# Kernel optimization log

Hardware: AMD Instinct MI355X
Metric: run time of the kernel (lower is better)

Reference implementation:

```python
import jax, jax.numpy as jnp
import numpy as np

DIM = 1024
N_HEADS = 16
B, T = 2, 2048


def setup_inputs() -> dict:
    key = jax.random.key(0)
    ks = jax.random.split(key, 9)
    s = 1.0 / np.sqrt(DIM)
    return {
        "x": jax.random.normal(ks[0], (B, T, DIM), dtype=jnp.float32),
        "Wq": jax.random.normal(ks[1], (DIM, DIM), dtype=jnp.float32) * s,
        "bq": jnp.zeros((DIM,), dtype=jnp.float32),
        "Wk": jax.random.normal(ks[2], (DIM, DIM), dtype=jnp.float32) * s,
        "bk": jnp.zeros((DIM,), dtype=jnp.float32),
        "Wv": jax.random.normal(ks[3], (DIM, DIM), dtype=jnp.float32) * s,
        "bv": jnp.zeros((DIM,), dtype=jnp.float32),
        "Wo": jax.random.normal(ks[4], (DIM, DIM), dtype=jnp.float32) * s,
        "bo": jnp.zeros((DIM,), dtype=jnp.float32),
    }


def reference(x, Wq, bq, Wk, bk, Wv, bv, Wo, bo):
    Bv, Tv, d = x.shape
    n = N_HEADS
    hd = d // n
    # projections (torch Linear: x @ W.T + b)
    Q = x @ Wq.T + bq
    K = x @ Wk.T + bk
    V = x @ Wv.T + bv
    # [B, n, T, hd]
    Q = Q.reshape(Bv, Tv, n, hd).transpose(0, 2, 1, 3)
    K = K.reshape(Bv, Tv, n, hd).transpose(0, 2, 1, 3)
    V = V.reshape(Bv, Tv, n, hd).transpose(0, 2, 1, 3)
    # NOTE: original scales by full model dim, not head dim
    scale = 1.0 / jnp.sqrt(jnp.asarray(d, dtype=x.dtype))
    scores = jnp.einsum('bnqd,bnkd->bnqk', Q, K) * scale
    causal = jnp.tril(jnp.ones((Tv, Tv), dtype=bool))
    scores = jnp.where(causal, scores, jnp.asarray(-jnp.inf, dtype=scores.dtype))
    attn = jax.nn.softmax(scores, axis=-1)
    out = jnp.einsum('bnqk,bnkd->bnqd', attn, V)
    out = out.transpose(0, 2, 1, 3).reshape(Bv, Tv, d)
    return out @ Wo.T + bo
```

## Files before the change

kernel.cpp:

```cpp
#include <hip/hip_runtime.h>
#include <math.h>

#define DIMN 1024
#define NH 16
#define HD 64
#define BATCH 2
#define SEQ 2048
#define MROWS (BATCH*SEQ)

typedef unsigned short u16;
typedef unsigned int u32;
typedef __attribute__((ext_vector_type(8))) short bf16x8;
typedef __attribute__((ext_vector_type(4))) float f32x4;

__device__ __forceinline__ u16 f2bf(float f) {
    unsigned u = __float_as_uint(f);
    u += 0x7FFF + ((u >> 16) & 1);
    return (u16)(u >> 16);
}
__device__ __forceinline__ float bf2f(u16 s) {
    return __uint_as_float(((unsigned)s) << 16);
}

#define GLOADLDS16(g, s)                                                     \
    __builtin_amdgcn_global_load_lds(                                        \
        (const __attribute__((address_space(1))) void*)(g),                  \
        (__attribute__((address_space(3))) void*)(s), 16, 0, 0)

__global__ __launch_bounds__(256)
void split_hilo(const float* __restrict__ src, u16* __restrict__ h,
                u16* __restrict__ l, int n4)
{
    int i = blockIdx.x * 256 + threadIdx.x;
    if (i >= n4) return;
    float4 v = ((const float4*)src)[i];
    ushort4 hv, lv;
    hv.x = f2bf(v.x); lv.x = f2bf(v.x - bf2f(hv.x));
    hv.y = f2bf(v.y); lv.y = f2bf(v.y - bf2f(hv.y));
    hv.z = f2bf(v.z); lv.z = f2bf(v.z - bf2f(hv.z));
    hv.w = f2bf(v.w); lv.w = f2bf(v.w - bf2f(hv.w));
    ((ushort4*)h)[i] = hv;
    ((ushort4*)l)[i] = lv;
}

__global__ __launch_bounds__(256)
void split4_hilo(const float* __restrict__ s0, const float* __restrict__ s1,
                 const float* __restrict__ s2, const float* __restrict__ s3,
                 u16* __restrict__ h0, u16* __restrict__ l0,
                 u16* __restrict__ h1, u16* __restrict__ l1,
                 u16* __restrict__ h2, u16* __restrict__ l2,
                 u16* __restrict__ h3, u16* __restrict__ l3, int n4)
{
    const float* src; u16* h; u16* l;
    switch (blockIdx.z) {
        case 0: src = s0; h = h0; l = l0; break;
        case 1: src = s1; h = h1; l = l1; break;
        case 2: src = s2; h = h2; l = l2; break;
        default: src = s3; h = h3; l = l3; break;
    }
    int i = blockIdx.x * 256 + threadIdx.x;
    if (i >= n4) return;
    float4 v = ((const float4*)src)[i];
    ushort4 hv, lv;
    hv.x = f2bf(v.x); lv.x = f2bf(v.x - bf2f(hv.x));
    hv.y = f2bf(v.y); lv.y = f2bf(v.y - bf2f(hv.y));
    hv.z = f2bf(v.z); lv.z = f2bf(v.z - bf2f(hv.z));
    hv.w = f2bf(v.w); lv.w = f2bf(v.w - bf2f(hv.w));
    ((ushort4*)h)[i] = hv;
    ((ushort4*)l)[i] = lv;
}

template<int NF, bool QKV>
__global__ __launch_bounds__(256)
void mfma_gemm(const u16* __restrict__ Ah, const u16* __restrict__ Al,
               const u16* __restrict__ Wh0, const u16* __restrict__ Wl0,
               const u16* __restrict__ Wh1, const u16* __restrict__ Wl1,
               const u16* __restrict__ Wh2, const u16* __restrict__ Wl2,
               const float* __restrict__ b0, const float* __restrict__ b1,
               const float* __restrict__ b2,
               u16* __restrict__ Qh, u16* __restrict__ Ql,
               u16* __restrict__ Kh, u16* __restrict__ Kl,
               float* __restrict__ Vw, float* __restrict__ Yout)
{
    constexpr int BM = 128;
    constexpr int BN = NF * 32;
    constexpr int BK = 32;
    __shared__ u16 AhS[BM*BK], AlS[BM*BK], WhS[BN*BK], WlS[BN*BK];

    const u16* Wh = Wh0; const u16* Wl = Wl0; const float* bias = b0;
    if (QKV) {
        if (blockIdx.z == 1)      { Wh = Wh1; Wl = Wl1; bias = b1; }
        else if (blockIdx.z == 2) { Wh = Wh2; Wl = Wl2; bias = b2; }
    }

    const int tid  = threadIdx.x;
    const int lane = tid & 63;
    const int wid  = tid >> 6;
    const int wr   = wid >> 1;
    const int wc   = wid & 1;

    const int m0 = blockIdx.x * BM;
    const int n0 = blockIdx.y * BN;

    const int srow = lane >> 2;
    const int skc  = (lane & 3) << 3;
    const int c0 = wid * 2, c1 = wid * 2 + 1;
    const size_t aoffg0 = (size_t)(m0 + c0*16 + srow) * DIMN + skc;
    const size_t aoffg1 = (size_t)(m0 + c1*16 + srow) * DIMN + skc;
    const size_t woffg0 = (size_t)(n0 + c0*16 + srow) * DIMN + skc;
    const size_t woffg1 = (size_t)(n0 + c1*16 + srow) * DIMN + skc;
    const bool doW = (c0 < BN/16);

    f32x4 acc[4][NF];
    #pragma unroll
    for (int m = 0; m < 4; ++m)
        #pragma unroll
        for (int n = 0; n < NF; ++n)
            acc[m][n] = (f32x4){0.f, 0.f, 0.f, 0.f};

    const int fr = lane & 15;
    const int fq = lane >> 4;
    const int aoff = (wr*64 + fr) * BK + fq*8;
    const int boff = (wc*(NF*16) + fr) * BK + fq*8;

    for (int k0 = 0; k0 < DIMN; k0 += BK) {
        GLOADLDS16(Ah + aoffg0 + k0, &AhS[c0*512]);
        GLOADLDS16(Ah + aoffg1 + k0, &AhS[c1*512]);
        GLOADLDS16(Al + aoffg0 + k0, &AlS[c0*512]);
        GLOADLDS16(Al + aoffg1 + k0, &AlS[c1*512]);
        if (doW) {
            GLOADLDS16(Wh + woffg0 + k0, &WhS[c0*512]);
            GLOADLDS16(Wh + woffg1 + k0, &WhS[c1*512]);
            GLOADLDS16(Wl + woffg0 + k0, &WlS[c0*512]);
            GLOADLDS16(Wl + woffg1 + k0, &WlS[c1*512]);
        }
        __syncthreads();

        bf16x8 ah[4], al[4], bh[NF], bl[NF];
        #pragma unroll
        for (int m = 0; m < 4; ++m) {
            ah[m] = *(const bf16x8*)&AhS[aoff + m*16*BK];
            al[m] = *(const bf16x8*)&AlS[aoff + m*16*BK];
        }
        #pragma unroll
        for (int n = 0; n < NF; ++n) {
            bh[n] = *(const bf16x8*)&WhS[boff + n*16*BK];
            bl[n] = *(const bf16x8*)&WlS[boff + n*16*BK];
        }
        #pragma unroll
        for (int m = 0; m < 4; ++m)
            #pragma unroll
            for (int n = 0; n < NF; ++n) {
                acc[m][n] = __builtin_amdgcn_mfma_f32_16x16x32_bf16(ah[m], bh[n], acc[m][n], 0, 0, 0);
                acc[m][n] = __builtin_amdgcn_mfma_f32_16x16x32_bf16(ah[m], bl[n], acc[m][n], 0, 0, 0);
                acc[m][n] = __builtin_amdgcn_mfma_f32_16x16x32_bf16(al[m], bh[n], acc[m][n], 0, 0, 0);
            }
        __syncthreads();
    }

    #pragma unroll
    for (int n = 0; n < NF; ++n) {
        const int col = n0 + wc*(NF*16) + n*16 + fr;
        const float bv = bias[col];
        #pragma unroll
        for (int m = 0; m < 4; ++m) {
            #pragma unroll
            for (int j = 0; j < 4; ++j) {
                const int row = m0 + wr*64 + m*16 + fq*4 + j;
                float v = acc[m][n][j] + bv;
                if (QKV) {
                    const int b_ = row >> 11, t = row & (SEQ - 1);
                    const int hh = col >> 6, d = col & 63;
                    const size_t rb = (((size_t)b_*NH + hh)*SEQ + t)*HD;
                    if (blockIdx.z == 0) {
                        v *= 0.03125f;
                        u16 hv = f2bf(v), lv = f2bf(v - bf2f(hv));
                        Qh[rb + d] = hv; Ql[rb + d] = lv;
                    } else if (blockIdx.z == 1) {
                        u16 hv = f2bf(v), lv = f2bf(v - bf2f(hv));
                        const int ds = d ^ ((t & 7) << 3);
                        Kh[rb + ds] = hv; Kl[rb + ds] = lv;
                    } else {
                        Vw[rb + d] = v;
                    }
                } else {
                    Yout[(size_t)row*DIMN + col] = v;
                }
            }
        }
    }
}

__global__ __launch_bounds__(256)
void convV(const float* __restrict__ Vw, u16* __restrict__ Vth, u16* __restrict__ Vtl)
{
    __shared__ float Vs[64][68];
    const int tid = threadIdx.x;
    const int bh = blockIdx.y;
    const int t0 = blockIdx.x * 64;
    const float* src = Vw + ((size_t)bh*SEQ + t0)*HD;
    #pragma unroll
    for (int k = 0; k < 4; ++k) {
        int f4 = tid + k*256;
        int r = f4 >> 4, c4 = (f4 & 15) << 2;
        *(float4*)&Vs[r][c4] = *(const float4*)(src + (size_t)r*HD + c4);
    }
    __syncthreads();
    const int d  = tid >> 2;
    const int q2 = (tid & 3) << 4;
    u16* oh = Vth + ((size_t)bh*HD + d)*SEQ + t0;
    u16* ol = Vtl + ((size_t)bh*HD + d)*SEQ + t0;
    #pragma unroll
    for (int p = 0; p < 4; ++p) {
        const int lt = q2 + p*4;
        const int t_sw = (lt & 32) | ((((lt >> 3) & 3) ^ (d & 3)) << 3) | (lt & 7);
        ushort4 hv, lv; float v;
        v = Vs[lt + 0][d]; hv.x = f2bf(v); lv.x = f2bf(v - bf2f(hv.x));
        v = Vs[lt + 1][d]; hv.y = f2bf(v); lv.y = f2bf(v - bf2f(hv.y));
        v = Vs[lt + 2][d]; hv.z = f2bf(v); lv.z = f2bf(v - bf2f(hv.z));
        v = Vs[lt + 3][d]; hv.w = f2bf(v); lv.w = f2bf(v - bf2f(hv.w));
        *(ushort4*)(oh + t_sw) = hv;
        *(ushort4*)(ol + t_sw) = lv;
    }
}

__global__ __launch_bounds__(256)
void attn_mfma(const u16* __restrict__ Qhg, const u16* __restrict__ Qlg,
               const u16* __restrict__ Khg, const u16* __restrict__ Klg,
               const u16* __restrict__ Vthg, const u16* __restrict__ Vtlg,
               u16* __restrict__ AH, u16* __restrict__ AL)
{
    __shared__ u16 KVS[2][4][2048];
    __shared__ u16 PhS[4][640];
    __shared__ u16 PlS[4][640];

    const int tid  = threadIdx.x;
    const int lane = tid & 63;
    const int w    = tid >> 6;
    const int fr   = lane & 15;
    const int fq   = lane >> 4;
    const int bh   = blockIdx.y;
    const int b_   = bh >> 4;
    const int h    = bh & 15;

    auto stage = [&](int buf, int kt2) {
        u16* dst = &KVS[buf][w][0];
        if (w < 2) {
            const u16* g = (w == 0 ? Khg : Klg) +
                ((size_t)bh*SEQ + (size_t)kt2*32 + (lane>>3))*HD + ((lane&7)<<3);
            #pragma unroll
            for (int i = 0; i < 4; ++i)
                GLOADLDS16(g + (size_t)i*8*HD, dst + i*512);
        } else {
            const u16* g = (w == 2 ? Vthg : Vtlg) +
                ((size_t)bh*HD + (lane>>2))*SEQ + (size_t)kt2*32 + ((lane&3)<<3);
            #pragma unroll
            for (int i = 0; i < 4; ++i)
                GLOADLDS16(g + (size_t)i*16*SEQ, dst + i*512);
        }
    };

    #pragma unroll 1
    for (int pass = 0; pass < 2; ++pass) {
        const int qt   = pass ? (31 - blockIdx.x) : blockIdx.x;
        const int qabs = qt*64 + w*16 + fr;
        const int nt   = 2*qt + 2;

        bf16x8 qh[2], ql[2];
        {
            const size_t qrow = ((size_t)bh*SEQ + qabs)*HD;
            #pragma unroll
            for (int ks = 0; ks < 2; ++ks) {
                qh[ks] = *(const bf16x8*)&Qhg[qrow + ks*32 + (fq<<3)];
                ql[ks] = *(const bf16x8*)&Qlg[qrow + ks*32 + (fq<<3)];
            }
        }

        f32x4 o[4];
        #pragma unroll
        for (int md = 0; md < 4; ++md) o[md] = (f32x4){0.f,0.f,0.f,0.f};
        float mrun = -INFINITY, lrun = 0.f;

        __syncthreads();
        stage(0, 0);
        int cur = 0;

        for (int kt = 0; kt < nt; ++kt) {
            __syncthreads();
            if (kt + 1 < nt) stage(cur ^ 1, kt + 1);

            f32x4 s0 = (f32x4){0.f,0.f,0.f,0.f};
            f32x4 s1 = (f32x4){0.f,0.f,0.f,0.f};
            __builtin_amdgcn_s_setprio(1);
            #pragma unroll
            for (int ks = 0; ks < 2; ++ks) {
                const int sl = (((ks*4 + fq) ^ (fr & 7)) << 3);
                bf16x8 a0h = *(const bf16x8*)&KVS[cur][0][fr*64 + sl];
                bf16x8 a0l = *(const bf16x8*)&KVS[cur][1][fr*64 + sl];
                bf16x8 a1h = *(const bf16x8*)&KVS[cur][0][(16+fr)*64 + sl];
                bf16x8 a1l = *(const bf16x8*)&KVS[cur][1][(16+fr)*64 + sl];
                s0 = __builtin_amdgcn_mfma_f32_16x16x32_bf16(a0h, qh[ks], s0, 0,0,0);
                s0 = __builtin_amdgcn_mfma_f32_16x16x32_bf16(a0h, ql[ks], s0, 0,0,0);
                s0 = __builtin_amdgcn_mfma_f32_16x16x32_bf16(a0l, qh[ks], s0, 0,0,0);
                s1 = __builtin_amdgcn_mfma_f32_16x16x32_bf16(a1h, qh[ks], s1, 0,0,0);
                s1 = __builtin_amdgcn_mfma_f32_16x16x32_bf16(a1h, ql[ks], s1, 0,0,0);
                s1 = __builtin_amdgcn_mfma_f32_16x16x32_bf16(a1l, qh[ks], s1, 0,0,0);
            }
            __builtin_amdgcn_s_setprio(0);

            const int kb = kt*32 + fq*4;
            #pragma unroll
            for (int j = 0; j < 4; ++j) {
                if (kb + j      > qabs) s0[j] = -INFINITY;
                if (kb + 16 + j > qabs) s1[j] = -INFINITY;
            }

            float pm = fmaxf(fmaxf(fmaxf(s0[0],s0[1]), fmaxf(s0[2],s0[3])),
                             fmaxf(fmaxf(s1[0],s1[1]), fmaxf(s1[2],s1[3])));
            pm = fmaxf(pm, __shfl_xor(pm, 16));
            pm = fmaxf(pm, __shfl_xor(pm, 32));

            if (!__all(pm - mrun <= 8.0f)) {
                const float mnew = fmaxf(mrun, pm);
                const float fac  = __expf(mrun - mnew);
                lrun *= fac;
                #pragma unroll
                for (int md = 0; md < 4; ++md) {
                    o[md][0] *= fac; o[md][1] *= fac;
                    o[md][2] *= fac; o[md][3] *= fac;
                }
                mrun = mnew;
            }
            float p[8];
            #pragma unroll
            for (int j = 0; j < 4; ++j) {
                p[j]   = __expf(s0[j] - mrun);
                p[4+j] = __expf(s1[j] - mrun);
            }
            float ls = ((p[0]+p[1]) + (p[2]+p[3])) + ((p[4]+p[5]) + (p[6]+p[7]));
            ls += __shfl_xor(ls, 16);
            ls += __shfl_xor(ls, 32);
            lrun += ls;

            u16 ph[8], pl[8];
            #pragma unroll
            for (int i = 0; i < 8; ++i) {
                ph[i] = f2bf(p[i]);
                pl[i] = f2bf(p[i] - bf2f(ph[i]));
            }
            {
                const int pb = fr*40 + fq*4;
                uint2 w0, w1;
                w0.x = (u32)ph[0] | ((u32)ph[1] << 16);
                w0.y = (u32)ph[2] | ((u32)ph[3] << 16);
                w1.x = (u32)ph[4] | ((u32)ph[5] << 16);
                w1.y = (u32)ph[6] | ((u32)ph[7] << 16);
                *(uint2*)&PhS[w][pb]      = w0;
                *(uint2*)&PhS[w][pb + 16] = w1;
                w0.x = (u32)pl[0] | ((u32)pl[1] << 16);
                w0.y = (u32)pl[2] | ((u32)pl[3] << 16);
                w1.x = (u32)pl[4] | ((u32)pl[5] << 16);
                w1.y = (u32)pl[6] | ((u32)pl[7] << 16);
                *(uint2*)&PlS[w][pb]      = w0;
                *(uint2*)&PlS[w][pb + 16] = w1;
            }

            bf16x8 bph = *(const bf16x8*)&PhS[w][fr*40 + (fq<<3)];
            bf16x8 bpl = *(const bf16x8*)&PlS[w][fr*40 + (fq<<3)];
            __builtin_amdgcn_s_setprio(1);
            #pragma unroll
            for (int md = 0; md < 4; ++md) {
                const int vsl = ((fq ^ (fr & 3)) << 3);
                bf16x8 avh = *(const bf16x8*)&KVS[cur][2][(md*16+fr)*32 + vsl];
                bf16x8 avl = *(const bf16x8*)&KVS[cur][3][(md*16+fr)*32 + vsl];
                o[md] = __builtin_amdgcn_mfma_f32_16x16x32_bf16(avh, bph, o[md], 0,0,0);
                o[md] = __builtin_amdgcn_mfma_f32_16x16x32_bf16(avh, bpl, o[md], 0,0,0);
                o[md] = __builtin_amdgcn_mfma_f32_16x16x32_bf16(avl, bph, o[md], 0,0,0);
            }
            __builtin_amdgcn_s_setprio(0);
            cur ^= 1;
        }

        const float inv = 1.f / lrun;
        const size_t ob = ((size_t)b_*SEQ + qabs)*DIMN + h*64;
        #pragma unroll
        for (int md = 0; md < 4; ++md) {
            #pragma unroll
            for (int pr = 0; pr < 2; ++pr) {
                const int d0 = md*16 + fq*4 + pr*2;
                const float v0 = o[md][pr*2]   * inv;
                const float v1 = o[md][pr*2+1] * inv;
                u16 h0 = f2bf(v0), l0 = f2bf(v0 - bf2f(h0));
                u16 h1 = f2bf(v1), l1 = f2bf(v1 - bf2f(h1));
                *(u32*)&AH[ob + d0] = (u32)h0 | ((u32)h1 << 16);
                *(u32*)&AL[ob + d0] = (u32)l0 | ((u32)l1 << 16);
            }
        }
    }
}

extern "C" void kernel_launch(void* const* d_in, const int* in_sizes, int n_in,
                              void* d_out, int out_size, void* d_ws, size_t ws_size,
                              hipStream_t stream)
{
    const float* x  = (const float*)d_in[0];
    const float* Wq = (const float*)d_in[1];
    const float* bq = (const float*)d_in[2];
    const float* Wk = (const float*)d_in[3];
    const float* bk = (const float*)d_in[4];
    const float* Wv = (const float*)d_in[5];
    const float* bv = (const float*)d_in[6];
    const float* Wo = (const float*)d_in[7];
    const float* bo = (const float*)d_in[8];
    float* out = (float*)d_out;

    const size_t NX = (size_t)MROWS * DIMN;
    const size_t NW = (size_t)DIMN * DIMN;

    u16* Xh  = (u16*)d_ws;
    u16* Xl  = Xh  + NX;
    u16* WhQ = Xl  + NX;  u16* WlQ = WhQ + NW;
    u16* WhK = WlQ + NW;  u16* WlK = WhK + NW;
    u16* WhV = WlK + NW;  u16* WlV = WhV + NW;
    u16* WhO = WlV + NW;  u16* WlO = WhO + NW;
    u16* Qh  = WlO + NW;
    u16* Ql  = Qh + NX;
    u16* Kh  = Ql + NX;
    u16* Kl  = Kh + NX;
    u16* Vth = Kl + NX;
    u16* Vtl = Vth + NX;
    float* Vw = (float*)(Vtl + NX);
    u16* AH = Xh;
    u16* AL = Xl;

    const int n4x = (int)(NX / 4);
    const int n4w = (int)(NW / 4);
    split_hilo<<<n4x/256, 256, 0, stream>>>(x, Xh, Xl, n4x);
    dim3 gs(n4w/256, 1, 4);
    split4_hilo<<<gs, 256, 0, stream>>>(Wq, Wk, Wv, Wo,
                                        WhQ, WlQ, WhK, WlK, WhV, WlV, WhO, WlO, n4w);

    dim3 gq(MROWS/128, DIMN/128, 3);
    mfma_gemm<4, true><<<gq, 256, 0, stream>>>(Xh, Xl, WhQ, WlQ, WhK, WlK, WhV, WlV,
                                               bq, bk, bv, Qh, Ql, Kh, Kl, Vw, nullptr);

    dim3 gv(SEQ / 64, BATCH * NH);
    convV<<<gv, 256, 0, stream>>>(Vw, Vth, Vtl);

    dim3 ga(16, BATCH * NH);
    attn_mfma<<<ga, 256, 0, stream>>>(Qh, Ql, Kh, Kl, Vth, Vtl, AH, AL);

    dim3 gp(MROWS/128, DIMN/64, 1);
    mfma_gemm<2, false><<<gp, 256, 0, stream>>>(AH, AL, WhO, WlO, nullptr, nullptr,
                                                nullptr, nullptr, bo, nullptr, nullptr,
                                                nullptr, nullptr, nullptr, nullptr,
                                                nullptr, out);
}
```

Baseline: 339.2 us.

## Merge split kernels, fold log2e into Q scale, remap attention blocks for XCD locality

The separate x and weight hi/lo split kernels become one five-slice launch, removing a kernel launch. The Q scale now includes log2(e), so softmax uses exp2f directly and the deferred-rescale threshold is adjusted to match. Attention block indices are remapped so blocks sharing a batch-head land on the same XCD, aiming at better L2 reuse of K/V. The bf16 conversion now uses the HIP intrinsic, and the merged split grid launches many idle blocks for the smaller weight slices.

```diff
diff --git a/kernel.cpp b/kernel.cpp
--- a/kernel.cpp
+++ b/kernel.cpp
@@ -1,4 +1,5 @@
 #include <hip/hip_runtime.h>
+#include <hip/hip_bf16.h>
 #include <math.h>
 
 #define DIMN 1024
@@ -13,10 +14,12 @@
 typedef __attribute__((ext_vector_type(8))) short bf16x8;
 typedef __attribute__((ext_vector_type(4))) float f32x4;
 
+#define QSCALE 0.0450842200279f
+#define DEFER_THR 11.5415603372f
+
 __device__ __forceinline__ u16 f2bf(float f) {
-    unsigned u = __float_as_uint(f);
-    u += 0x7FFF + ((u >> 16) & 1);
-    return (u16)(u >> 16);
+    __hip_bfloat16 h = __float2bfloat16(f);
+    return *reinterpret_cast<u16*>(&h);
 }
 __device__ __forceinline__ float bf2f(u16 s) {
     return __uint_as_float(((unsigned)s) << 16);
@@ -28,35 +31,23 @@
         (__attribute__((address_space(3))) void*)(s), 16, 0, 0)
 
 __global__ __launch_bounds__(256)
-void split_hilo(const float* __restrict__ src, u16* __restrict__ h,
-                u16* __restrict__ l, int n4)
-{
-    int i = blockIdx.x * 256 + threadIdx.x;
-    if (i >= n4) return;
-    float4 v = ((const float4*)src)[i];
-    ushort4 hv, lv;
-    hv.x = f2bf(v.x); lv.x = f2bf(v.x - bf2f(hv.x));
-    hv.y = f2bf(v.y); lv.y = f2bf(v.y - bf2f(hv.y));
-    hv.z = f2bf(v.z); lv.z = f2bf(v.z - bf2f(hv.z));
-    hv.w = f2bf(v.w); lv.w = f2bf(v.w - bf2f(hv.w));
-    ((ushort4*)h)[i] = hv;
-    ((ushort4*)l)[i] = lv;
-}
-
-__global__ __launch_bounds__(256)
-void split4_hilo(const float* __restrict__ s0, const float* __restrict__ s1,
+void split5_hilo(const float* __restrict__ s0, const float* __restrict__ s1,
                  const float* __restrict__ s2, const float* __restrict__ s3,
+                 const float* __restrict__ s4,
                  u16* __restrict__ h0, u16* __restrict__ l0,
                  u16* __restrict__ h1, u16* __restrict__ l1,
                  u16* __restrict__ h2, u16* __restrict__ l2,
-                 u16* __restrict__ h3, u16* __restrict__ l3, int n4)
+                 u16* __restrict__ h3, u16* __restrict__ l3,
+                 u16* __restrict__ h4, u16* __restrict__ l4,
+                 int n4x, int n4w)
 {
-    const float* src; u16* h; u16* l;
+    const float* src; u16* h; u16* l; int n4;
     switch (blockIdx.z) {
-        case 0: src = s0; h = h0; l = l0; break;
-        case 1: src = s1; h = h1; l = l1; break;
-        case 2: src = s2; h = h2; l = l2; break;
-        default: src = s3; h = h3; l = l3; break;
+        case 0: src = s0; h = h0; l = l0; n4 = n4x; break;
+        case 1: src = s1; h = h1; l = l1; n4 = n4w; break;
+        case 2: src = s2; h = h2; l = l2; n4 = n4w; break;
+        case 3: src = s3; h = h3; l = l3; n4 = n4w; break;
+        default: src = s4; h = h4; l = l4; n4 = n4w; break;
     }
     int i = blockIdx.x * 256 + threadIdx.x;
     if (i >= n4) return;
@@ -173,7 +164,7 @@
                     const int hh = col >> 6, d = col & 63;
                     const size_t rb = (((size_t)b_*NH + hh)*SEQ + t)*HD;
                     if (blockIdx.z == 0) {
-                        v *= 0.03125f;
+                        v *= QSCALE;
                         u16 hv = f2bf(v), lv = f2bf(v - bf2f(hv));
                         Qh[rb + d] = hv; Ql[rb + d] = lv;
                     } else if (blockIdx.z == 1) {
@@ -239,9 +230,14 @@
     const int w    = tid >> 6;
     const int fr   = lane & 15;
     const int fq   = lane >> 4;
-    const int bh   = blockIdx.y;
-    const int b_   = bh >> 4;
-    const int h    = bh & 15;
+
+    const int lin = blockIdx.y * 16 + blockIdx.x;
+    const int xcd = lin & 7;
+    const int idx = lin >> 3;
+    const int bh  = (xcd << 2) | (idx & 3);
+    const int qtp = idx >> 2;
+    const int b_  = bh >> 4;
+    const int h   = bh & 15;
 
     auto stage = [&](int buf, int kt2) {
         u16* dst = &KVS[buf][w][0];
@@ -262,7 +258,7 @@
 
     #pragma unroll 1
     for (int pass = 0; pass < 2; ++pass) {
-        const int qt   = pass ? (31 - blockIdx.x) : blockIdx.x;
+        const int qt   = pass ? (31 - qtp) : qtp;
         const int qabs = qt*64 + w*16 + fr;
         const int nt   = 2*qt + 2;
 
@@ -320,9 +316,9 @@
             pm = fmaxf(pm, __shfl_xor(pm, 16));
             pm = fmaxf(pm, __shfl_xor(pm, 32));
 
-            if (!__all(pm - mrun <= 8.0f)) {
+            if (!__all(pm - mrun <= DEFER_THR)) {
                 const float mnew = fmaxf(mrun, pm);
-                const float fac  = __expf(mrun - mnew);
+                const float fac  = exp2f(mrun - mnew);
                 lrun *= fac;
                 #pragma unroll
                 for (int md = 0; md < 4; ++md) {
@@ -334,8 +330,8 @@
             float p[8];
             #pragma unroll
             for (int j = 0; j < 4; ++j) {
-                p[j]   = __expf(s0[j] - mrun);
-                p[4+j] = __expf(s1[j] - mrun);
+                p[j]   = exp2f(s0[j] - mrun);
+                p[4+j] = exp2f(s1[j] - mrun);
             }
             float ls = ((p[0]+p[1]) + (p[2]+p[3])) + ((p[4]+p[5]) + (p[6]+p[7]));
             ls += __shfl_xor(ls, 16);
@@ -435,10 +431,10 @@
 
     const int n4x = (int)(NX / 4);
     const int n4w = (int)(NW / 4);
-    split_hilo<<<n4x/256, 256, 0, stream>>>(x, Xh, Xl, n4x);
-    dim3 gs(n4w/256, 1, 4);
-    split4_hilo<<<gs, 256, 0, stream>>>(Wq, Wk, Wv, Wo,
-                                        WhQ, WlQ, WhK, WlK, WhV, WlV, WhO, WlO, n4w);
+    dim3 gs(n4x/256, 1, 5);
+    split5_hilo<<<gs, 256, 0, stream>>>(x, Wq, Wk, Wv, Wo,
+                                        Xh, Xl, WhQ, WlQ, WhK, WlK, WhV, WlV,
+                                        WhO, WlO, n4x, n4w);
 
     dim3 gq(MROWS/128, DIMN/128, 3);
     mfma_gemm<4, true><<<gq, 256, 0, stream>>>(Xh, Xl, WhQ, WlQ, WhK, WlK, WhV, WlV,
```

Measured after the change: 327.6 us. 1.04x faster.
